# Performance work log

Hardware: AMD Instinct MI355X
Metric: run time of the kernel (lower is better)

Reference implementation:

```python
import jax, jax.numpy as jnp
import numpy as np

B, S, D, H = 4, 1024, 1024, 16
HS = D // H  # head_size = 64


def setup_inputs() -> dict:
    key = jax.random.key(0)
    ks = jax.random.split(key, 6)
    scale = 1.0 / np.sqrt(D)
    data = jax.random.normal(ks[0], (B, S, D), dtype=jnp.float32)
    # Per-head projection weights, stacked: [H, D, HS] (no bias, per nn.Linear(bias=False))
    Wq = jax.random.normal(ks[1], (H, D, HS), dtype=jnp.float32) * scale
    Wk = jax.random.normal(ks[2], (H, D, HS), dtype=jnp.float32) * scale
    Wv = jax.random.normal(ks[3], (H, D, HS), dtype=jnp.float32) * scale
    # Output projection: [H*HS, D] plus bias [D]
    Wo = jax.random.normal(ks[4], (H * HS, D), dtype=jnp.float32) * scale
    bo = jax.random.normal(ks[5], (D,), dtype=jnp.float32) * 0.01
    return {"data": data, "Wq": Wq, "Wk": Wk, "Wv": Wv, "Wo": Wo, "bo": bo}


def reference(data, Wq, Wk, Wv, Wo, bo):
    b, s, d = data.shape
    # Per-head Q/K/V projections (self-attention: encoder_data = data)
    q = jnp.einsum('bsd,hde->bhse', data, Wq)  # [B,H,S,HS]
    k = jnp.einsum('bsd,hde->bhse', data, Wk)
    v = jnp.einsum('bsd,hde->bhse', data, Wv)
    # NOTE: original scales by sqrt(embedding_dimension), not sqrt(head_size)
    scores = jnp.einsum('bhse,bhte->bhst', q, k) / jnp.sqrt(jnp.asarray(d, dtype=data.dtype))
    # causal mask (tril of block_size, sliced to [S, S])
    causal = jnp.tril(jnp.ones((s, s), dtype=bool))
    scores = jnp.where(causal, scores, -jnp.inf)
    attn = jax.nn.softmax(scores, axis=-1)  # dropout rate 0.0 -> identity
    out = jnp.einsum('bhst,bhte->bhse', attn, v)  # [B,H,S,HS]
    # concat heads along feature dim (head order matches ModuleList order)
    out = out.transpose(0, 2, 1, 3).reshape(b, s, -1)  # [B,S,H*HS]
    return out @ Wo + bo
```

## Files before the change

kernel.cpp:

```cpp
#include <hip/hip_runtime.h>
#include <hip/hip_bf16.h>
#include <stdint.h>

#define NEG_SENTINEL (-1e30f)

typedef short s16x8 __attribute__((ext_vector_type(8)));
typedef float f32x4 __attribute__((ext_vector_type(4)));
typedef float f32x16 __attribute__((ext_vector_type(16)));
typedef unsigned int uint32x2 __attribute__((ext_vector_type(2)));

__device__ __forceinline__ ushort f2bf(float f) {
  union { float f; uint32_t u; } v; v.f = f;
  uint32_t u = v.u;
  u += 0x7fffu + ((u >> 16) & 1u);
  return (ushort)(u >> 16);
}
__device__ __forceinline__ ushort f2bf_rn(float f) {
  union { float f; uint32_t u; } v; v.f = f;
  return (ushort)((v.u + 0x8000u) >> 16);
}

__device__ __forceinline__ uint32_t pk_bf16(float lo, float hi) {
  uint32_t r;
  asm("v_cvt_pk_bf16_f32 %0, %1, %2" : "=v"(r) : "v"(lo), "v"(hi));
  return r;
}

__device__ __forceinline__ void async_ld16(ushort* lds, const ushort* g) {
  __builtin_amdgcn_global_load_lds(
      (const __attribute__((address_space(1))) uint32_t*)g,
      (__attribute__((address_space(3))) uint32_t*)lds, 16, 0, 0);
}

__global__ __launch_bounds__(256) void prep_all(
    const float* __restrict__ data, const float* __restrict__ Wq,
    const float* __restrict__ Wk, const float* __restrict__ Wv,
    const float* __restrict__ Wo, ushort* __restrict__ dataB,
    ushort* __restrict__ WTall, ushort* __restrict__ WoT) {
  const int g = blockIdx.x;
  const int tid = threadIdx.x;
  __shared__ __align__(16) ushort tile[64 * 72];

  if (g < 2048) {
    long i = ((long)g * 256 + tid) * 8;
    float4 a = *(const float4*)(data + i);
    float4 b = *(const float4*)(data + i + 4);
    union { ushort u[8]; uint4 v; } o;
    o.u[0] = f2bf(a.x); o.u[1] = f2bf(a.y); o.u[2] = f2bf(a.z); o.u[3] = f2bf(a.w);
    o.u[4] = f2bf(b.x); o.u[5] = f2bf(b.y); o.u[6] = f2bf(b.z); o.u[7] = f2bf(b.w);
    *(uint4*)(dataB + i) = o.v;
    return;
  }

  if (g < 2816) {
    const int u = g - 2048;
    const int z = u >> 4, it = u & 15;
    const int matsel = z >> 4;
    const float* src = (matsel == 0 ? Wq : (matsel == 1 ? Wk : Wv)) +
                       (long)(z & 15) * 65536;
    ushort* dst = WTall + (long)z * 65536;
#pragma unroll
    for (int p = 0; p < 4; ++p) {
      int chunk = tid + p * 256;
      int r = chunk >> 4, c0 = (chunk & 15) * 4;
      float4 f = *(const float4*)(src + (long)(it * 64 + r) * 64 + c0);
      union { ushort u2[4]; uint2 v; } o;
      o.u2[0] = f2bf(f.x); o.u2[1] = f2bf(f.y);
      o.u2[2] = f2bf(f.z); o.u2[3] = f2bf(f.w);
      *(uint2*)&tile[r * 72 + c0] = o.v;
    }
    __syncthreads();
#pragma unroll
    for (int p = 0; p < 2; ++p) {
      int chunk = tid + p * 256;
      int r = chunk >> 3, c0 = (chunk & 7) * 8;
      union { ushort u2[8]; uint4 v; } tmp;
#pragma unroll
      for (int k2 = 0; k2 < 8; ++k2) tmp.u2[k2] = tile[(c0 + k2) * 72 + r];
      *(uint4*)(dst + (long)r * 1024 + it * 64 + c0) = tmp.v;
    }
    return;
  }

  {
    const int u = g - 2816;
    const int jt = u & 15, it = u >> 4;
#pragma unroll
    for (int p = 0; p < 4; ++p) {
      int chunk = tid + p * 256;
      int r = chunk >> 4, c0 = (chunk & 15) * 4;
      float4 f = *(const float4*)(Wo + (long)(it * 64 + r) * 1024 + jt * 64 + c0);
      union { ushort u2[4]; uint2 v; } o;
      o.u2[0] = f2bf(f.x); o.u2[1] = f2bf(f.y);
      o.u2[2] = f2bf(f.z); o.u2[3] = f2bf(f.w);
      *(uint2*)&tile[r * 72 + c0] = o.v;
    }
    __syncthreads();
#pragma unroll
    for (int p = 0; p < 2; ++p) {
      int chunk = tid + p * 256;
      int r = chunk >> 3, c0 = (chunk & 7) * 8;
      union { ushort u2[8]; uint4 v; } tmp;
#pragma unroll
      for (int k2 = 0; k2 < 8; ++k2) tmp.u2[k2] = tile[(c0 + k2) * 72 + r];
      *(uint4*)(WoT + (long)(jt * 64 + r) * 1024 + it * 64 + c0) = tmp.v;
    }
  }
}

#define BAR() do { asm volatile("" ::: "memory"); \
  __builtin_amdgcn_s_barrier(); \
  asm volatile("" ::: "memory"); } while (0)
#define LGKM0() do { asm volatile("s_waitcnt lgkmcnt(0)" ::: "memory"); \
  __builtin_amdgcn_sched_barrier(0); } while (0)
#define STAGE2(LDSB, G) do { \
  async_ld16((LDSB) + o0, (G) + so0); \
  async_ld16((LDSB) + o0 + 4096, (G) + so0 + 65536); } while (0)
#define LD_A(PA, MIB) do { \
  _Pragma("unroll") for (int dm = 0; dm < 4; ++dm) { \
    afr[dm][0] = *(const s16x8*)((PA) + ((MIB) + dm) * 1024); \
    afr[dm][1] = *(const s16x8*)((PA) + ((MIB) + dm) * 1024 + 512); } } while (0)
#define LD_B(PB, NIB) do { \
  _Pragma("unroll") for (int dn = 0; dn < 2; ++dn) { \
    bfr[(NIB) + dn][0] = *(const s16x8*)((PB) + ((NIB) + dn) * 1024); \
    bfr[(NIB) + dn][1] = *(const s16x8*)((PB) + ((NIB) + dn) * 1024 + 512); } } while (0)
#define MFMA_Q(MIB, NIB) do { \
  __builtin_amdgcn_s_setprio(1); \
  _Pragma("unroll") for (int kg = 0; kg < 2; ++kg) \
    _Pragma("unroll") for (int dm = 0; dm < 4; ++dm) \
      _Pragma("unroll") for (int dn = 0; dn < 2; ++dn) \
        acc[(MIB) + dm][(NIB) + dn] = __builtin_amdgcn_mfma_f32_16x16x32_bf16( \
            afr[dm][kg], bfr[(NIB) + dn][kg], acc[(MIB) + dm][(NIB) + dn], 0, 0, 0); \
  __builtin_amdgcn_s_setprio(0); } while (0)

__global__ __launch_bounds__(512, 1) void qkv_proj256(
    const ushort* __restrict__ dataB, const ushort* __restrict__ WTall,
    ushort* __restrict__ QKV) {
  __shared__ __align__(16) ushort smem[65536];
  const int tid = threadIdx.x;
  const int lane = tid & 63, w = tid >> 6, quad = lane >> 4, l15 = lane & 15;
  const int wm = w >> 2, wn = w & 3;
  const int m0 = blockIdx.x * 256;
  const int n0 = blockIdx.y * 256;

  const int o0 = tid * 8;
  const int st_ = o0 >> 9, u_ = o0 & 511;
  const int u0_ = u_ ^ (((u_ >> 8) & 1) << 4);
  const long so0 = (long)((st_ >> 1) * 16 + (u0_ >> 5)) * 1024 +
                   (st_ & 1) * 32 + (u0_ & 31);

  const ushort* Ab = dataB + (long)m0 * 1024;
  const ushort* Bb = WTall + (long)n0 * 1024;

  const int alane = (l15 * 32 + quad * 8) ^ (((l15 >> 3) & 1) << 4);
  const ushort* pA0 = smem + wm * 8192 + alane;
  const ushort* pB0 = smem + 16384 + (wn >> 1) * 8192 + (wn & 1) * 4096 + alane;
  const ushort* pA1 = pA0 + 32768;
  const ushort* pB1 = pB0 + 32768;

  f32x4 acc[8][4];
  const f32x4 z = {0.f, 0.f, 0.f, 0.f};
#pragma unroll
  for (int mi = 0; mi < 8; ++mi)
#pragma unroll
    for (int ni = 0; ni < 4; ++ni) acc[mi][ni] = z;

  s16x8 afr[4][2];
  s16x8 bfr[4][2];

  STAGE2(smem + 16384, Bb);
  STAGE2(smem + 16384 + 8192, Bb + 131072);
  STAGE2(smem, Ab);
  STAGE2(smem + 8192, Ab + 131072);
  STAGE2(smem + 32768 + 16384, Bb + 64);
  STAGE2(smem + 32768 + 16384 + 8192, Bb + 131072 + 64);
  asm volatile("s_waitcnt vmcnt(4)" ::: "memory");
  BAR();

#pragma unroll 1
  for (int it = 0; it < 8; ++it) {
    const int t0k = it * 128;
    const bool sN = (it < 7);
    LD_A(pA0, 0); LD_B(pB0, 0);
    STAGE2(smem + 32768, Ab + t0k + 64);
    asm volatile("s_waitcnt lgkmcnt(8)" ::: "memory");
    BAR(); LGKM0();
    MFMA_Q(0, 0);
    BAR();
    LD_B(pB0, 2);
    STAGE2(smem + 32768 + 8192, Ab + 131072 + t0k + 64);
    BAR(); LGKM0();
    MFMA_Q(0, 2);
    BAR();
    LD_A(pA0, 4);
    if (sN) STAGE2(smem + 16384, Bb + t0k + 128);
    BAR(); LGKM0();
    MFMA_Q(4, 0);
    BAR();
    if (sN) STAGE2(smem + 16384 + 8192, Bb + 131072 + t0k + 128);
    BAR(); LGKM0();
    MFMA_Q(4, 2);
    if (sN) { asm volatile("s_waitcnt vmcnt(4)" ::: "memory"); }
    else    { asm volatile("s_waitcnt vmcnt(0)" ::: "memory"); }
    BAR();
    LD_A(pA1, 0); LD_B(pB1, 0);
    if (sN) STAGE2(smem, Ab + t0k + 128);
    asm volatile("s_waitcnt lgkmcnt(8)" ::: "memory");
    BAR(); LGKM0();
    MFMA_Q(0, 0);
    BAR();
    LD_B(pB1, 2);
    if (sN) STAGE2(smem + 8192, Ab + 131072 + t0k + 128);
    BAR(); LGKM0();
    MFMA_Q(0, 2);
    BAR();
    LD_A(pA1, 4);
    if (sN) STAGE2(smem + 32768 + 16384, Bb + t0k + 192);
    BAR(); LGKM0();
    MFMA_Q(4, 0);
    BAR();
    if (sN) STAGE2(smem + 32768 + 16384 + 8192, Bb + 131072 + t0k + 192);
    BAR(); LGKM0();
    MFMA_Q(4, 2);
    if (sN) {
      asm volatile("s_waitcnt vmcnt(4)" ::: "memory");
      BAR();
    }
  }

  const int matsel = n0 >> 10;
  const int bI = m0 >> 10, s0 = m0 & 1023;
  const int nloc0 = (n0 & 1023) + wn * 64;
  if (matsel < 2) {
    const float sc = (matsel == 0) ? 0.04508422f : 1.0f;
    ushort* base = QKV + (long)matsel * 4194304 + (long)bI * 1048576;
#pragma unroll
    for (int mi = 0; mi < 8; ++mi) {
#pragma unroll
      for (int ni = 0; ni < 4; ++ni) {
        int n = nloc0 + ni * 16 + l15;
        int h = n >> 6, e = n & 63;
        int sb = s0 + wm * 128 + mi * 16 + quad * 4;
        ushort* p = base + (long)h * 65536 + (sb >> 5) * 2048 + (e >> 4) * 512 +
                    ((e >> 3) & 1) * 256 + (sb & 31) * 8 + (e & 7);
#pragma unroll
        for (int i = 0; i < 4; ++i)
          p[i * 8] = f2bf(acc[mi][ni][i] * sc);
      }
    }
  } else {
    ushort* base = QKV + 8388608 + (long)bI * 1048576;
#pragma unroll
    for (int mi = 0; mi < 8; ++mi) {
#pragma unroll
      for (int ni = 0; ni < 4; ++ni) {
        int n = nloc0 + ni * 16 + l15;
        int h = n >> 6, e = n & 63;
        int sb = s0 + wm * 128 + mi * 16 + quad * 4;
        union { ushort u[4]; uint2 v; } o;
#pragma unroll
        for (int i = 0; i < 4; ++i) o.u[i] = f2bf(acc[mi][ni][i]);
        *(uint2*)(base + (long)h * 65536 + (sb >> 5) * 2048 +
                  ((e >> 5) + 2 * ((sb >> 4) & 1)) * 512 +
                  ((e & 31) + 32 * ((sb >> 3) & 1)) * 8 + (sb & 7)) = o.v;
      }
    }
  }
}

__global__ __launch_bounds__(512, 1) void out_proj(
    const ushort* __restrict__ Ocat, const ushort* __restrict__ WoT,
    const float* __restrict__ bo, float* __restrict__ out) {
  __shared__ __align__(16) ushort As[2][8192];
  __shared__ __align__(16) ushort Bs[2][8192];
  const int m0 = blockIdx.x * 128;
  const int n0 = blockIdx.y * 128;
  const int tid = threadIdx.x;
  const int lane = tid & 63, w = tid >> 6, quad = lane >> 4, l15 = lane & 15;
  const int wm = w >> 2, wn = w & 3;
  const ushort* A = Ocat + (long)m0 * 1024;
  const ushort* BT = WoT + (long)n0 * 1024;

  const int o0 = tid * 8;
  const int st_ = o0 >> 9, u_ = o0 & 511;
  const int u0_ = u_ ^ (((u_ >> 8) & 1) << 4);
  const long so0 = (long)((st_ >> 1) * 16 + (u0_ >> 5)) * 1024 +
                   (st_ & 1) * 32 + (u0_ & 31);

  const int alane = (l15 * 32 + quad * 8) ^ (((l15 >> 3) & 1) << 4);

  f32x4 acc[4][2];
  const f32x4 z = {0.f, 0.f, 0.f, 0.f};
#pragma unroll
  for (int mi = 0; mi < 4; ++mi)
#pragma unroll
    for (int ni = 0; ni < 2; ++ni) acc[mi][ni] = z;

  async_ld16(&As[0][o0], A + so0);
  async_ld16(&As[0][o0 + 4096], A + so0 + 65536);
  async_ld16(&Bs[0][o0], BT + so0);
  async_ld16(&Bs[0][o0 + 4096], BT + so0 + 65536);
  __syncthreads();

#pragma unroll 1
  for (int t = 0; t < 16; ++t) {
    const int cur = t & 1;
    if (t < 15) {
      const int k0 = (t + 1) * 64;
      async_ld16(&As[cur ^ 1][o0], A + k0 + so0);
      async_ld16(&As[cur ^ 1][o0 + 4096], A + k0 + so0 + 65536);
      async_ld16(&Bs[cur ^ 1][o0], BT + k0 + so0);
      async_ld16(&Bs[cur ^ 1][o0 + 4096], BT + k0 + so0 + 65536);
    }
    const ushort* pA = &As[cur][alane];
    const ushort* pB = &Bs[cur][alane];
#pragma unroll
    for (int kg = 0; kg < 2; ++kg) {
      s16x8 af[4], bfr[2];
#pragma unroll
      for (int mi = 0; mi < 4; ++mi)
        af[mi] = *(const s16x8*)(pA + (wm * 8 + mi * 2 + kg) * 512);
#pragma unroll
      for (int ni = 0; ni < 2; ++ni)
        bfr[ni] = *(const s16x8*)(pB + (wn * 4 + ni * 2 + kg) * 512);
#pragma unroll
      for (int mi = 0; mi < 4; ++mi)
#pragma unroll
        for (int ni = 0; ni < 2; ++ni)
          acc[mi][ni] = __builtin_amdgcn_mfma_f32_16x16x32_bf16(
              af[mi], bfr[ni], acc[mi][ni], 0, 0, 0);
    }
    __syncthreads();
  }

#pragma unroll
  for (int mi = 0; mi < 4; ++mi) {
#pragma unroll
    for (int ni = 0; ni < 2; ++ni) {
#pragma unroll
      for (int i = 0; i < 4; ++i) {
        int m = m0 + wm * 64 + mi * 16 + quad * 4 + i;
        int n = n0 + wn * 32 + ni * 16 + l15;
        out[(long)m * 1024 + n] = acc[mi][ni][i] + bo[n];
      }
    }
  }
}

#define LOAD_KV(KF, VF, S) do { \
  _Pragma("unroll") for (int es = 0; es < 4; ++es) \
    KF[es] = *(const s16x8*)(Kp + (S) * 2048 + es * 512 + lane * 8); \
  _Pragma("unroll") for (int t = 0; t < 4; ++t) \
    VF[t] = *(const s16x8*)(VTp + (S) * 2048 + t * 512 + lane * 8); } while (0)

#define ATTN_STEP(KF, VF, S) do { \
  f32x16 sacc; \
  _Pragma("unroll") for (int r = 0; r < 16; ++r) sacc[r] = 0.f; \
  __builtin_amdgcn_s_setprio(1); \
  _Pragma("unroll") for (int es = 0; es < 4; ++es) \
    sacc = __builtin_amdgcn_mfma_f32_32x32x16_bf16(KF[es], qf[es], sacc, 0, 0, 0); \
  __builtin_amdgcn_s_setprio(0); \
  if ((S) == c) { \
    _Pragma("unroll") for (int r = 0; r < 16; ++r) { \
      int kvoff = (r & 3) + 8 * (r >> 2) + 4 * hi; \
      if (kvoff > l31) sacc[r] = NEG_SENTINEL; \
    } \
  } \
  float ex[16]; \
  _Pragma("unroll") for (int r = 0; r < 16; ++r) { \
    ex[r] = exp2f(sacc[r]); l_part += ex[r]; } \
  uint32_t xw[8]; \
  _Pragma("unroll") for (int k = 0; k < 8; ++k) \
    xw[k] = pk_bf16(ex[2 * k], ex[2 * k + 1]); \
  _Pragma("unroll") for (int win = 0; win < 2; ++win) { \
    const int bs = 4 * win; \
    uint32x2 sw0 = __builtin_amdgcn_permlane32_swap(xw[bs + 0], xw[bs + 2], \
                                                    false, false); \
    uint32x2 sw1 = __builtin_amdgcn_permlane32_swap(xw[bs + 1], xw[bs + 3], \
                                                    false, false); \
    union { uint32_t u[4]; s16x8 v; } pa; \
    pa.u[0] = sw0[0]; pa.u[1] = sw1[0]; pa.u[2] = sw0[1]; pa.u[3] = sw1[1]; \
    __builtin_amdgcn_s_setprio(1); \
    oacc0 = __builtin_amdgcn_mfma_f32_32x32x16_bf16(pa.v, VF[win * 2 + 0], \
                                                    oacc0, 0, 0, 0); \
    oacc1 = __builtin_amdgcn_mfma_f32_32x32x16_bf16(pa.v, VF[win * 2 + 1], \
                                                    oacc1, 0, 0, 0); \
    __builtin_amdgcn_s_setprio(0); \
  } } while (0)

__global__ __launch_bounds__(512, 1) void attn_kernel(
    const ushort* __restrict__ QKV, ushort* __restrict__ Ocat) {
  const int x = blockIdx.x;
  const int tid = threadIdx.x;
  const int w = tid >> 6;
  const int lane = tid & 63, l31 = lane & 31, hi = lane >> 5;
  const int c = (w < 4) ? (31 - (x >> 4)) : (x >> 4);
  const int bh = (x & 15) * 4 + (w & 3);
  const int b = bh >> 4, h = bh & 15;
  const int q0 = c * 32;

  const ushort* Qp = QKV + (long)bh * 65536;
  const ushort* Kp = QKV + 4194304 + (long)bh * 65536;
  const ushort* VTp = QKV + 8388608 + (long)bh * 65536;

  s16x8 qf[4];
#pragma unroll
  for (int es = 0; es < 4; ++es)
    qf[es] = *(const s16x8*)(Qp + c * 2048 + es * 512 + lane * 8);

  f32x16 oacc0, oacc1;
#pragma unroll
  for (int r = 0; r < 16; ++r) { oacc0[r] = 0.f; oacc1[r] = 0.f; }
  float l_part = 0.f;
  const int nsub = c + 1;

  s16x8 kc[4], vc[4], kn[4], vn[4];
  LOAD_KV(kc, vc, 0);

  int s = 0;
  while (true) {
    bool last = (s + 1 >= nsub);
    if (!last) LOAD_KV(kn, vn, s + 1);
    ATTN_STEP(kc, vc, s);
    if (last) break;
    ++s;
    last = (s + 1 >= nsub);
    if (!last) LOAD_KV(kc, vc, s + 1);
    ATTN_STEP(kn, vn, s);
    if (last) break;
    ++s;
  }

  float l_tot = l_part + __shfl_xor(l_part, 32, 64);

  ushort* Ob = Ocat + ((long)(b * 1024 + q0) * 1024) + h * 64;
#pragma unroll
  for (int r = 0; r < 16; ++r) {
    int qloc = (r & 3) + 8 * (r >> 2) + 4 * hi;
    float lv = __shfl(l_tot, qloc, 64);
    float linv = __builtin_amdgcn_rcpf(lv > 1e-30f ? lv : 1.0f);
    Ob[(long)qloc * 1024 + l31] = f2bf_rn(oacc0[r] * linv);
    Ob[(long)qloc * 1024 + 32 + l31] = f2bf_rn(oacc1[r] * linv);
  }
}

extern "C" void kernel_launch(void* const* d_in, const int* in_sizes, int n_in,
                              void* d_out, int out_size, void* d_ws, size_t ws_size,
                              hipStream_t stream) {
  const float* data = (const float*)d_in[0];
  const float* Wq = (const float*)d_in[1];
  const float* Wk = (const float*)d_in[2];
  const float* Wv = (const float*)d_in[3];
  const float* Wo = (const float*)d_in[4];
  const float* bo = (const float*)d_in[5];
  float* out = (float*)d_out;

  ushort* ws = (ushort*)d_ws;
  ushort* QKV = ws;
  ushort* dataB = ws + 12582912;
  ushort* Ocat = ws + 16777216;
  ushort* WTall = ws + 20971520;
  ushort* WoT = ws + 20971520 + 3145728;

  prep_all<<<dim3(3072), dim3(256), 0, stream>>>(data, Wq, Wk, Wv, Wo,
                                                 dataB, WTall, WoT);
  qkv_proj256<<<dim3(16, 12), dim3(512), 0, stream>>>(dataB, WTall, QKV);
  attn_kernel<<<dim3(256), dim3(512), 0, stream>>>(QKV, Ocat);
  out_proj<<<dim3(32, 8), dim3(512), 0, stream>>>(Ocat, WoT, bo, out);
}
```

Baseline: 160.5 us.

## Triple-buffer out_proj loads and remap workgroups for L2 locality

The output projection moves from a double-buffered to a triple-buffered async load pipeline that prefetches two k-tiles ahead. It uses explicit vmcnt waits instead of draining all loads at each barrier, so more global-load latency can overlap with MFMA work. Both GEMM kernels also remap block IDs so that consecutive workgroups, likely resident on different XCDs, get grouped tiles, aiming to improve L2 reuse. This raises out_proj shared memory use and assumes the grid shape in the hard-coded swizzle constants.

```diff
diff --git a/kernel.cpp b/kernel.cpp
--- a/kernel.cpp
+++ b/kernel.cpp
@@ -140,8 +140,10 @@
   const int tid = threadIdx.x;
   const int lane = tid & 63, w = tid >> 6, quad = lane >> 4, l15 = lane & 15;
   const int wm = w >> 2, wn = w & 3;
-  const int m0 = blockIdx.x * 256;
-  const int n0 = blockIdx.y * 256;
+  const int bid = blockIdx.x + (blockIdx.y << 4);
+  const int wg = (bid & 7) * 24 + (bid >> 3);
+  const int m0 = (wg & 15) * 256;
+  const int n0 = (wg >> 4) * 256;
 
   const int o0 = tid * 8;
   const int st_ = o0 >> 9, u_ = o0 & 511;
@@ -271,13 +273,15 @@
 __global__ __launch_bounds__(512, 1) void out_proj(
     const ushort* __restrict__ Ocat, const ushort* __restrict__ WoT,
     const float* __restrict__ bo, float* __restrict__ out) {
-  __shared__ __align__(16) ushort As[2][8192];
-  __shared__ __align__(16) ushort Bs[2][8192];
-  const int m0 = blockIdx.x * 128;
-  const int n0 = blockIdx.y * 128;
+  __shared__ __align__(16) ushort As[3][8192];
+  __shared__ __align__(16) ushort Bs[3][8192];
   const int tid = threadIdx.x;
   const int lane = tid & 63, w = tid >> 6, quad = lane >> 4, l15 = lane & 15;
   const int wm = w >> 2, wn = w & 3;
+  const int bid = blockIdx.x + (blockIdx.y << 5);
+  const int wg = (bid & 7) * 32 + (bid >> 3);
+  const int m0 = (wg & 31) * 128;
+  const int n0 = (wg >> 5) * 128;
   const ushort* A = Ocat + (long)m0 * 1024;
   const ushort* BT = WoT + (long)n0 * 1024;
 
@@ -296,21 +300,23 @@
 #pragma unroll
     for (int ni = 0; ni < 2; ++ni) acc[mi][ni] = z;
 
-  async_ld16(&As[0][o0], A + so0);
-  async_ld16(&As[0][o0 + 4096], A + so0 + 65536);
-  async_ld16(&Bs[0][o0], BT + so0);
-  async_ld16(&Bs[0][o0 + 4096], BT + so0 + 65536);
-  __syncthreads();
-
+#define OP_STAGE(BUF, K0) do { \
+  async_ld16(&As[BUF][o0], A + (K0) + so0); \
+  async_ld16(&As[BUF][o0 + 4096], A + (K0) + so0 + 65536); \
+  async_ld16(&Bs[BUF][o0], BT + (K0) + so0); \
+  async_ld16(&Bs[BUF][o0 + 4096], BT + (K0) + so0 + 65536); } while (0)
+
+  OP_STAGE(0, 0);
+  OP_STAGE(1, 64);
+  asm volatile("s_waitcnt vmcnt(4)" ::: "memory");
+  BAR();
+
+  int cur = 0;
 #pragma unroll 1
   for (int t = 0; t < 16; ++t) {
-    const int cur = t & 1;
-    if (t < 15) {
-      const int k0 = (t + 1) * 64;
-      async_ld16(&As[cur ^ 1][o0], A + k0 + so0);
-      async_ld16(&As[cur ^ 1][o0 + 4096], A + k0 + so0 + 65536);
-      async_ld16(&Bs[cur ^ 1][o0], BT + k0 + so0);
-      async_ld16(&Bs[cur ^ 1][o0 + 4096], BT + k0 + so0 + 65536);
+    if (t < 14) {
+      const int nxt = (cur + 2 >= 3) ? cur - 1 : cur + 2;
+      OP_STAGE(nxt, (t + 2) * 64);
     }
     const ushort* pA = &As[cur][alane];
     const ushort* pB = &Bs[cur][alane];
@@ -330,8 +336,12 @@
           acc[mi][ni] = __builtin_amdgcn_mfma_f32_16x16x32_bf16(
               af[mi], bfr[ni], acc[mi][ni], 0, 0, 0);
     }
-    __syncthreads();
-  }
+    if (t < 14)      { asm volatile("s_waitcnt vmcnt(4)" ::: "memory"); }
+    else if (t == 14){ asm volatile("s_waitcnt vmcnt(0)" ::: "memory"); }
+    if (t < 15) BAR();
+    cur = (cur + 1 >= 3) ? 0 : cur + 1;
+  }
+#undef OP_STAGE
 
 #pragma unroll
   for (int mi = 0; mi < 4; ++mi) {
```

Result: slower. 166.4 us (+3.7%).
